# Kernel optimization log

Hardware: AMD Instinct MI355X
Metric: run time of the kernel (lower is better)

Reference implementation:

```python
import jax, jax.numpy as jnp
import numpy as np


def setup_inputs() -> dict:
    key = jax.random.key(0)
    k0, k1, k2, k3 = jax.random.split(key, 4)
    B, T, Din, H, Dout = 8, 4096, 1024, 1024, 1024
    x = jax.random.normal(k0, (B, T, Din), dtype=jnp.float32)
    # Linear weights stored torch-style as [out_features, in_features]
    W_hg = jax.random.normal(k1, (2 * H, Din), dtype=jnp.float32) * 0.02
    W_out = jax.random.normal(k2, (Dout, H), dtype=jnp.float32) * 0.02
    # episode-reset flags, 0/1 floats, shape [B,T,1] (expanded over channels)
    is_init = jax.random.bernoulli(k3, 0.01, (B, T, 1)).astype(jnp.float32)
    h_0 = jnp.zeros((B, 1, H), dtype=jnp.float32)
    return {"x": x, "W_hg": W_hg, "W_out": W_out, "is_init": is_init, "h_0": h_0}


def _mingru_scan(gate, hidden, is_init, h_0):
    # Linear recurrence h_t = (1-g_t) h_{t-1} + g_t * hidden_t, with resets.
    A = 1.0 - gate               # [B,T,H]
    Bv = gate * hidden           # [B,T,H]
    r = jnp.broadcast_to(is_init, Bv.shape)

    def combine(c1, c2):
        a1, b1, r1 = c1
        a2, b2, r2 = c2
        reset = r2 > 0
        a = jnp.where(reset, a2, a2 * a1)
        b = jnp.where(reset, b2, a2 * b1 + b2)
        return a, b, jnp.minimum(r1 + r2, 1.0)  # clamp(max=1)

    # Prepending the identity element then dropping it (as the torch code does)
    # is a no-op for an inclusive associative scan, so scan T elements directly.
    A_out, B_out, _ = jax.lax.associative_scan(combine, (A, Bv, r), axis=1)
    return A_out * h_0 + B_out   # h_0 is [B,1,H], broadcasts over T


def reference(x, W_hg, W_out, is_init, h_0):
    hg = jnp.einsum("btd,hd->bth", x, W_hg)          # [B,T,2H]
    hidden, gate = jnp.split(hg, 2, axis=-1)
    gate = jax.nn.sigmoid(gate)
    h = _mingru_scan(gate, hidden, is_init, h_0)      # [B,T,H]
    h_n = h[:, -1:]                                   # [B,1,H]
    out = jnp.einsum("bth,oh->bto", h, W_out)         # [B,T,Dout]
    return out, h_n
```

## Files before the change

kernel.cpp:

```cpp
#include <hip/hip_runtime.h>
#include <stdint.h>

#define B_DIM 8
#define T_DIM 4096
#define K_DIM 1024
#define H_DIM 1024
#define M_DIM (B_DIM * T_DIM)
#define CHUNK 64
#define NCHUNK (T_DIM / CHUNK)

typedef __attribute__((ext_vector_type(8))) short s16x8;
typedef __attribute__((ext_vector_type(4))) float f32x4;

__device__ __forceinline__ unsigned short f2b(float f) {
    union { float f; uint32_t u; } c; c.f = f;
    uint32_t r = (c.u + 0x7fffu + ((c.u >> 16) & 1u)) >> 16;
    return (unsigned short)r;
}
__device__ __forceinline__ float b2f(unsigned short u) {
    union { uint32_t u; float f; } c; c.u = ((uint32_t)u) << 16;
    return c.f;
}

__device__ __forceinline__ void gload_lds16(const unsigned short* g,
                                            unsigned short* l) {
    __builtin_amdgcn_global_load_lds(
        (__attribute__((address_space(1))) void*)g,
        (__attribute__((address_space(3))) void*)l, 16, 0, 0);
}

__device__ __forceinline__ void bar() {
    asm volatile("s_barrier" ::: "memory");
}


__global__ void cvt_f32_bf16(const float* __restrict__ src,
                             unsigned short* __restrict__ dst, int n4) {
    int stride = gridDim.x * blockDim.x;
    for (int i = blockIdx.x * blockDim.x + threadIdx.x; i < n4; i += stride) {
        float4 v = ((const float4*)src)[i];
        ushort4 o;
        o.x = f2b(v.x); o.y = f2b(v.y); o.z = f2b(v.z); o.w = f2b(v.w);
        ((ushort4*)dst)[i] = o;
    }
}

__global__ void prep_whg(const float* __restrict__ W,
                         unsigned short* __restrict__ Wp) {
    int i = blockIdx.x * blockDim.x + threadIdx.x;
    int total = 2 * H_DIM * K_DIM / 4;
    if (i >= total) return;
    int e = i * 4;
    int n = e >> 10;
    int k = e & 1023;
    int src = (n & 1) ? (H_DIM + (n >> 1)) : (n >> 1);
    float4 v = *(const float4*)&W[(size_t)src * K_DIM + k];
    ushort4 o;
    o.x = f2b(v.x); o.y = f2b(v.y); o.z = f2b(v.z); o.w = f2b(v.w);
    *(ushort4*)&Wp[(size_t)n * K_DIM + k] = o;
}


template <int EPI>
__global__ __launch_bounds__(512, 2) void gemm256(
    const unsigned short* __restrict__ A,
    const unsigned short* __restrict__ Bm,
    float* __restrict__ C,
    uint32_t* __restrict__ Sab,
    int N) {
    __shared__ unsigned short As4[4][256 * 32];
    __shared__ unsigned short Bs4[4][256 * 32];
    const int K = K_DIM;
    const int KT = K / 64;

    const int gx = gridDim.x;
    const int nwg = gx * gridDim.y;
    const int orig = blockIdx.y * gx + blockIdx.x;
    const int cpx = nwg >> 3;
    const int wg = (orig & 7) * cpx + (orig >> 3);
    const int m0 = (wg / gx) * 256;
    const int n0 = (wg % gx) * 256;

    const int t = threadIdx.x;
    const int lane = t & 63;
    const int w = t >> 6;
    const int wm = w >> 2, wn = w & 3;

    const int srow = lane & 15;
    const int sq   = lane >> 4;

    const int l15 = lane & 15;
    const int rq = lane >> 4;

    f32x4 acc[8][4];
#pragma unroll
    for (int m = 0; m < 8; m++)
#pragma unroll
        for (int n = 0; n < 4; n++) acc[m][n] = (f32x4){0.f, 0.f, 0.f, 0.f};

    auto stA = [&](int kt, int ks, int j) {
        const int slot = (2 * kt + ks) & 3;
        const int row = j * 128 + w * 16 + srow;
        const int gk  = kt * 64 + ks * 32 + sq * 8;
        gload_lds16(&A[(size_t)(m0 + row) * K + gk],
                    &As4[slot][(j * 128 + w * 16) * 32]);
    };
    auto stB = [&](int kt, int ks, int j) {
        const int slot = (2 * kt + ks) & 3;
        const int row = j * 128 + w * 16 + srow;
        const int gk  = kt * 64 + ks * 32 + sq * 8;
        gload_lds16(&Bm[(size_t)(n0 + row) * K + gk],
                    &Bs4[slot][(j * 128 + w * 16) * 32]);
    };

    s16x8 af[4], bf[4];

#define LDAX(S, MI) \
    (*(const s16x8*)&As4[S][(wm * 8 + (MI)) * 512 + rq * 128 + l15 * 8])
#define LDBX(S, NI) \
    (*(const s16x8*)&Bs4[S][(wn * 4 + (NI)) * 512 + rq * 128 + l15 * 8])

#define LGKM0 do { asm volatile("s_waitcnt lgkmcnt(0)" ::: "memory"); \
                   __builtin_amdgcn_sched_barrier(0); } while (0)
#define VMW6 asm volatile("s_waitcnt vmcnt(6)" ::: "memory")
#define VMW8 asm volatile("s_waitcnt vmcnt(8)" ::: "memory")
#define VMW0 asm volatile("s_waitcnt vmcnt(0)" ::: "memory")
#define NOPX ((void)0)

#define STA(KT_, KS_) do { stA((KT_), (KS_), 0); stA((KT_), (KS_), 1); } while (0)
#define STB(KT_, KS_) do { stB((KT_), (KS_), 0); stB((KT_), (KS_), 1); } while (0)

#define MFMA16(MB) do {                                                     \
    __builtin_amdgcn_s_setprio(1);                                          \
    _Pragma("unroll") for (int m_ = 0; m_ < 4; m_++)                        \
        _Pragma("unroll") for (int n_ = 0; n_ < 4; n_++)                    \
            acc[(MB) + m_][n_] = __builtin_amdgcn_mfma_f32_16x16x32_bf16(   \
                af[m_], bf[n_], acc[(MB) + m_][n_], 0, 0, 0);               \
    __builtin_amdgcn_s_setprio(0);                                          \
} while (0)

#define TILE(T_, ST1, ST2, ST3, ST4, VM2, VM4) do {                         \
    const int s0_ = (2 * (T_)) & 3, s1_ = (2 * (T_) + 1) & 3;               \
    _Pragma("unroll") for (int m_ = 0; m_ < 4; m_++) af[m_] = LDAX(s0_, m_);\
    _Pragma("unroll") for (int n_ = 0; n_ < 4; n_++) bf[n_] = LDBX(s0_, n_);\
    ST1;                                                                    \
    bar(); LGKM0; MFMA16(0); bar();                                         \
    _Pragma("unroll") for (int m_ = 0; m_ < 4; m_++) af[m_] = LDAX(s0_, m_ + 4); \
    ST2; VM2;                                                               \
    bar(); LGKM0; MFMA16(4); bar();                                         \
    _Pragma("unroll") for (int m_ = 0; m_ < 4; m_++) af[m_] = LDAX(s1_, m_);\
    _Pragma("unroll") for (int n_ = 0; n_ < 4; n_++) bf[n_] = LDBX(s1_, n_);\
    ST3;                                                                    \
    bar(); LGKM0; MFMA16(0); bar();                                         \
    _Pragma("unroll") for (int m_ = 0; m_ < 4; m_++) af[m_] = LDAX(s1_, m_ + 4); \
    ST4; VM4;                                                               \
    bar(); LGKM0; MFMA16(4); bar();                                         \
} while (0)

    STA(0, 0); STB(0, 0);
    STA(0, 1); STB(0, 1);
    STA(1, 0); STB(1, 0);
    VMW8;
    bar();

    for (int kt = 0; kt < KT - 2; ++kt) {
        TILE(kt, STA(kt + 1, 1), STB(kt + 1, 1),
                 STA(kt + 2, 0), STB(kt + 2, 0), VMW6, VMW6);
    }
    TILE(KT - 2, STA(KT - 1, 1), STB(KT - 1, 1), NOPX, NOPX, VMW6, VMW0);
    TILE(KT - 1, NOPX, NOPX, NOPX, NOPX, NOPX, NOPX);

    const int lr4 = rq * 4;
#pragma unroll
    for (int m = 0; m < 8; m++) {
#pragma unroll
        for (int n = 0; n < 4; n++) {
#pragma unroll
            for (int r = 0; r < 4; r++) {
                const int row = m0 + wm * 128 + m * 16 + lr4 + r;
                const int col = n0 + wn * 64 + n * 16 + l15;
                float v = acc[m][n][r];
                if (EPI == 0) {
                    C[(size_t)row * N + col] = v;
                } else {
                    float o = __shfl_xor(v, 1);
                    if ((lane & 1) == 0) {
                        float g = 1.f / (1.f + __expf(-o));
                        uint32_t pk = (uint32_t)f2b(1.f - g) |
                                      ((uint32_t)f2b(g * v) << 16);
                        Sab[(size_t)row * H_DIM + (col >> 1)] = pk;
                    }
                }
            }
        }
    }
#undef LDAX
#undef LDBX
#undef TILE
#undef MFMA16
#undef STA
#undef STB
}


__global__ __launch_bounds__(256) void scan_chunks(
    const uint32_t* __restrict__ Sab, const float* __restrict__ is_init,
    float* __restrict__ CA, float* __restrict__ CB, float* __restrict__ CR) {
    int idx = blockIdx.x * 256 + threadIdx.x;
    int ch = idx & (H_DIM - 1);
    int chunk = (idx >> 10) & (NCHUNK - 1);
    int b = idx >> 16;
    int t0 = chunk * CHUNK;
    size_t base = ((size_t)b * T_DIM + t0) * H_DIM + ch;
    const float* ii = is_init + (size_t)b * T_DIM + t0;
    float A = 1.f, Bv = 0.f;
    int rf = 0;
    for (int i = 0; i < CHUNK; i++) {
        uint32_t d = Sab[base + (size_t)i * H_DIM];
        float a = b2f((unsigned short)(d & 0xffffu));
        float bb = b2f((unsigned short)(d >> 16));
        bool rst = ii[i] > 0.f;
        A = rst ? a : a * A;
        Bv = rst ? bb : fmaf(a, Bv, bb);
        rf |= (int)rst;
    }
    size_t o = ((size_t)b * NCHUNK + chunk) * H_DIM + ch;
    CA[o] = A;
    CB[o] = Bv;
    if (ch == 0) CR[b * NCHUNK + chunk] = (float)rf;
}

__global__ void scan_tops(const float* __restrict__ CA, const float* __restrict__ CB,
                          const float* __restrict__ CR,
                          float* __restrict__ PA, float* __restrict__ PB) {
    int idx = blockIdx.x * blockDim.x + threadIdx.x;
    if (idx >= B_DIM * H_DIM) return;
    int ch = idx & (H_DIM - 1);
    int b = idx >> 10;
    float A = 1.f, Bv = 0.f;
    for (int c = 0; c < NCHUNK; c++) {
        size_t o = ((size_t)b * NCHUNK + c) * H_DIM + ch;
        PA[o] = A;
        PB[o] = Bv;
        float a = CA[o], bb = CB[o];
        bool rst = CR[b * NCHUNK + c] > 0.f;
        float nA = rst ? a : a * A;
        float nB = rst ? bb : fmaf(a, Bv, bb);
        A = nA; Bv = nB;
    }
}

__global__ __launch_bounds__(256) void scan_apply(
    const uint32_t* __restrict__ Sab, const float* __restrict__ is_init,
    const float* __restrict__ PA, const float* __restrict__ PB,
    const float* __restrict__ h0,
    unsigned short* __restrict__ hb, float* __restrict__ hn) {
    int idx = blockIdx.x * 256 + threadIdx.x;
    int ch = idx & (H_DIM - 1);
    int chunk = (idx >> 10) & (NCHUNK - 1);
    int b = idx >> 16;
    int t0 = chunk * CHUNK;
    size_t base = ((size_t)b * T_DIM + t0) * H_DIM + ch;
    const float* ii = is_init + (size_t)b * T_DIM + t0;
    size_t po = ((size_t)b * NCHUNK + chunk) * H_DIM + ch;
    float A = PA[po], Bv = PB[po];
    float h0v = h0[b * H_DIM + ch];
    float h = 0.f;
    for (int i = 0; i < CHUNK; i++) {
        uint32_t d = Sab[base + (size_t)i * H_DIM];
        float a = b2f((unsigned short)(d & 0xffffu));
        float bb = b2f((unsigned short)(d >> 16));
        bool rst = ii[i] > 0.f;
        A = rst ? a : a * A;
        Bv = rst ? bb : fmaf(a, Bv, bb);
        h = fmaf(A, h0v, Bv);
        hb[base + (size_t)i * H_DIM] = f2b(h);
    }
    if (chunk == NCHUNK - 1) hn[b * H_DIM + ch] = h;
}


extern "C" void kernel_launch(void* const* d_in, const int* in_sizes, int n_in,
                              void* d_out, int out_size, void* d_ws, size_t ws_size,
                              hipStream_t stream) {
    const float* x       = (const float*)d_in[0];
    const float* W_hg    = (const float*)d_in[1];
    const float* W_out   = (const float*)d_in[2];
    const float* is_init = (const float*)d_in[3];
    const float* h0      = (const float*)d_in[4];
    float* out = (float*)d_out;
    float* hn  = out + (size_t)M_DIM * H_DIM;

    char* ws = (char*)d_ws;
    size_t off = 0;
    auto alloc = [&](size_t bytes) {
        void* p = ws + off;
        off += (bytes + 255) & ~(size_t)255;
        return p;
    };
    unsigned short* xb  = (unsigned short*)alloc((size_t)M_DIM * K_DIM * 2);
    unsigned short* Wp  = (unsigned short*)alloc((size_t)2 * H_DIM * K_DIM * 2);
    unsigned short* Wob = (unsigned short*)alloc((size_t)H_DIM * K_DIM * 2);
    uint32_t* Sab = (uint32_t*)alloc((size_t)M_DIM * H_DIM * 4);
    float* CA = (float*)alloc((size_t)B_DIM * NCHUNK * H_DIM * 4);
    float* CB = (float*)alloc((size_t)B_DIM * NCHUNK * H_DIM * 4);
    float* CR = (float*)alloc((size_t)B_DIM * NCHUNK * 4);
    float* PA = (float*)alloc((size_t)B_DIM * NCHUNK * H_DIM * 4);
    float* PB = (float*)alloc((size_t)B_DIM * NCHUNK * H_DIM * 4);
    unsigned short* hb = xb;

    cvt_f32_bf16<<<2048, 256, 0, stream>>>(x, xb, M_DIM * K_DIM / 4);
    prep_whg<<<(2 * H_DIM * K_DIM / 4 + 255) / 256, 256, 0, stream>>>(W_hg, Wp);
    cvt_f32_bf16<<<1024, 256, 0, stream>>>(W_out, Wob, H_DIM * K_DIM / 4);

    gemm256<1><<<dim3(2048 / 256, M_DIM / 256), 512, 0, stream>>>(
        xb, Wp, nullptr, Sab, 2048);

    scan_chunks<<<(B_DIM * NCHUNK * H_DIM) / 256, 256, 0, stream>>>(
        Sab, is_init, CA, CB, CR);
    scan_tops<<<(B_DIM * H_DIM + 255) / 256, 256, 0, stream>>>(CA, CB, CR, PA, PB);
    scan_apply<<<(B_DIM * NCHUNK * H_DIM) / 256, 256, 0, stream>>>(
        Sab, is_init, PA, PB, h0, hb, hn);

    gemm256<0><<<dim3(1024 / 256, M_DIM / 256), 512, 0, stream>>>(
        hb, Wob, out, nullptr, 1024);
}
```

Baseline: 422.4 us.

## Restructure GEMM LDS pipeline to prefetch one full k-tile ahead

Changes the software pipeline of the bf16 MFMA GEMM so each k-tile iteration prefetches both halves of the next k-tile, instead of staging one half-tile further ahead. The vmcnt waits now sit after each second MFMA block rather than before it. The explicit lgkmcnt(0)+sched_barrier fences are removed, which leaves LDS-read wait placement to the compiler. This shortens the prologue and simplifies the loop tail, but global-load latency is hidden by fewer in-flight loads, and the compiler's scheduling may now interleave differently.

```diff
diff --git a/kernel.cpp b/kernel.cpp
--- a/kernel.cpp
+++ b/kernel.cpp
@@ -90,7 +90,7 @@
     const int sq   = lane >> 4;
 
     const int l15 = lane & 15;
-    const int rq = lane >> 4;
+    const int rq  = lane >> 4;
 
     f32x4 acc[8][4];
 #pragma unroll
@@ -120,10 +120,7 @@
 #define LDBX(S, NI) \
     (*(const s16x8*)&Bs4[S][(wn * 4 + (NI)) * 512 + rq * 128 + l15 * 8])
 
-#define LGKM0 do { asm volatile("s_waitcnt lgkmcnt(0)" ::: "memory"); \
-                   __builtin_amdgcn_sched_barrier(0); } while (0)
-#define VMW6 asm volatile("s_waitcnt vmcnt(6)" ::: "memory")
-#define VMW8 asm volatile("s_waitcnt vmcnt(8)" ::: "memory")
+#define VMW4 asm volatile("s_waitcnt vmcnt(4)" ::: "memory")
 #define VMW0 asm volatile("s_waitcnt vmcnt(0)" ::: "memory")
 #define NOPX ((void)0)
 
@@ -139,36 +136,34 @@
     __builtin_amdgcn_s_setprio(0);                                          \
 } while (0)
 
-#define TILE(T_, ST1, ST2, ST3, ST4, VM2, VM4) do {                         \
+#define TILE(T_, S1, S2, S3, S4, W2, W4) do {                               \
     const int s0_ = (2 * (T_)) & 3, s1_ = (2 * (T_) + 1) & 3;               \
     _Pragma("unroll") for (int m_ = 0; m_ < 4; m_++) af[m_] = LDAX(s0_, m_);\
     _Pragma("unroll") for (int n_ = 0; n_ < 4; n_++) bf[n_] = LDBX(s0_, n_);\
-    ST1;                                                                    \
-    bar(); LGKM0; MFMA16(0); bar();                                         \
+    S1;                                                                     \
+    bar(); MFMA16(0); bar();                                                \
     _Pragma("unroll") for (int m_ = 0; m_ < 4; m_++) af[m_] = LDAX(s0_, m_ + 4); \
-    ST2; VM2;                                                               \
-    bar(); LGKM0; MFMA16(4); bar();                                         \
+    S2;                                                                     \
+    bar(); MFMA16(4); W2; bar();                                            \
     _Pragma("unroll") for (int m_ = 0; m_ < 4; m_++) af[m_] = LDAX(s1_, m_);\
     _Pragma("unroll") for (int n_ = 0; n_ < 4; n_++) bf[n_] = LDBX(s1_, n_);\
-    ST3;                                                                    \
-    bar(); LGKM0; MFMA16(0); bar();                                         \
+    S3;                                                                     \
+    bar(); MFMA16(0); bar();                                                \
     _Pragma("unroll") for (int m_ = 0; m_ < 4; m_++) af[m_] = LDAX(s1_, m_ + 4); \
-    ST4; VM4;                                                               \
-    bar(); LGKM0; MFMA16(4); bar();                                         \
+    S4;                                                                     \
+    bar(); MFMA16(4); W4; bar();                                            \
 } while (0)
 
     STA(0, 0); STB(0, 0);
     STA(0, 1); STB(0, 1);
-    STA(1, 0); STB(1, 0);
-    VMW8;
+    VMW4;
     bar();
 
-    for (int kt = 0; kt < KT - 2; ++kt) {
-        TILE(kt, STA(kt + 1, 1), STB(kt + 1, 1),
-                 STA(kt + 2, 0), STB(kt + 2, 0), VMW6, VMW6);
-    }
-    TILE(KT - 2, STA(KT - 1, 1), STB(KT - 1, 1), NOPX, NOPX, VMW6, VMW0);
-    TILE(KT - 1, NOPX, NOPX, NOPX, NOPX, NOPX, NOPX);
+    for (int kt = 0; kt < KT - 1; ++kt) {
+        TILE(kt, STA(kt + 1, 0), STB(kt + 1, 0),
+                 STA(kt + 1, 1), STB(kt + 1, 1), VMW4, VMW4);
+    }
+    TILE(KT - 1, NOPX, NOPX, NOPX, NOPX, VMW0, NOPX);
 
     const int lr4 = rq * 4;
 #pragma unroll
```

Result: slower. 457.3 us (+8.3%).
